# Kernel tuning notes

Hardware: AMD Instinct MI355X
Metric: run time of the kernel (lower is better)

Reference implementation:

```python
import jax, jax.numpy as jnp
import numpy as np

IN_F = 4096
OUT_F = 11008
GROUPSIZE = 128
N_GROUPS = IN_F // GROUPSIZE  # 32


def setup_inputs() -> dict:
    key = jax.random.key(0)
    k1, k2, k3, k4 = jax.random.split(key, 4)
    x = jax.random.normal(k1, (4, 2048, IN_F), dtype=jnp.float32)
    # packed 4-bit weights: 8 nibbles per int32 along the input dim
    qweight = jax.random.randint(k2, (IN_F // 8, OUT_F), 0, 2**31 - 1, dtype=jnp.int32)
    # packed 4-bit zero points: 8 nibbles per int32 along the output dim
    qzeros = jax.random.randint(k3, (N_GROUPS, OUT_F // 8), 0, 2**31 - 1, dtype=jnp.int32)
    scales = jax.random.uniform(k4, (N_GROUPS, OUT_F), dtype=jnp.float32,
                                minval=0.001, maxval=0.01)
    g_idx = (jnp.arange(IN_F, dtype=jnp.int32) // GROUPSIZE).astype(jnp.int32)
    return {"x": x, "qweight": qweight, "scales": scales,
            "qzeros": qzeros, "g_idx": g_idx}


def _dequantize(qweight, scales, qzeros, g_idx):
    """GPTQ v2 dequant: W[i, j] = scales[g_idx[i], j] * (q[i, j] - (z[g_idx[i], j] + 1))."""
    shifts = jnp.arange(8, dtype=jnp.int32) * 4  # nibble shift amounts
    # unpack weights along input dim: [in/8, 8, out] -> [in, out]
    q = (qweight[:, None, :] >> shifts[None, :, None]) & 0xF
    q = q.reshape(-1, qweight.shape[1]).astype(scales.dtype)
    # unpack zeros along output dim: [g, out/8, 8] -> [g, out]; +1 per GPTQ v2
    z = ((qzeros[:, :, None] >> shifts[None, None, :]) & 0xF) + 1
    z = z.reshape(qzeros.shape[0], -1).astype(scales.dtype)
    return scales[g_idx] * (q - z[g_idx])  # [in, out]


def reference(x, qweight, scales, qzeros, g_idx):
    W = _dequantize(qweight, scales, qzeros, g_idx)  # [IN_F, OUT_F]
    return jnp.einsum('bsi,io->bso', x, W)
```

## Files before the change

kernel.cpp:

```cpp
#include <hip/hip_runtime.h>
#include <hip/hip_bf16.h>

#define IN_F 4096
#define OUT_F 11008

typedef __bf16 bf16_t;
typedef bf16_t bf16x8 __attribute__((ext_vector_type(8)));
typedef float f32x4 __attribute__((ext_vector_type(4)));
typedef unsigned int u32;

__global__ __launch_bounds__(256) void cvt_x_kernel(const float* __restrict__ x,
                                                    bf16_t* __restrict__ xb) {
    size_t i = ((size_t)blockIdx.x * 256 + threadIdx.x) * 8;
    f32x4 v0 = *(const f32x4*)(x + i);
    f32x4 v1 = *(const f32x4*)(x + i + 4);
    bf16x8 h;
    h[0]=(bf16_t)v0[0]; h[1]=(bf16_t)v0[1]; h[2]=(bf16_t)v0[2]; h[3]=(bf16_t)v0[3];
    h[4]=(bf16_t)v1[0]; h[5]=(bf16_t)v1[1]; h[6]=(bf16_t)v1[2]; h[7]=(bf16_t)v1[3];
    *(bf16x8*)(xb + i) = h;
}

__global__ __launch_bounds__(256) void dequant_kernel(const int* __restrict__ qweight,
                                                      const float* __restrict__ scales,
                                                      const int* __restrict__ qzeros,
                                                      bf16_t* __restrict__ wt) {
    const int n   = blockIdx.x * 256 + threadIdx.x;
    const int kw0 = blockIdx.y * 4;
    const int g   = kw0 >> 4;
    const float s  = scales[(size_t)g * OUT_F + n];
    const int   zw = qzeros[(size_t)g * (OUT_F / 8) + (n >> 3)];
    const float nsz = -s * (float)(((zw >> ((n & 7) * 4)) & 0xF) + 1);
    bf16_t* dst = wt + (size_t)n * IN_F + kw0 * 8;
    #pragma unroll
    for (int j = 0; j < 4; ++j) {
        const int w = qweight[(size_t)(kw0 + j) * OUT_F + n];
        bf16x8 h;
        #pragma unroll
        for (int b = 0; b < 8; ++b)
            h[b] = (bf16_t)fmaf((float)((w >> (4 * b)) & 0xF), s, nsz);
        *(bf16x8*)(dst + j * 8) = h;
    }
}


#define NI (IN_F / 128)

__global__ __launch_bounds__(512, 2) void gemm_8ph(const bf16_t* __restrict__ A,
                                                   const bf16_t* __restrict__ B,
                                                   float* __restrict__ C) {
    __shared__ __align__(16) bf16_t smemA[2 * 2 * 128 * 64];
    __shared__ __align__(16) bf16_t smemB[2 * 2 * 128 * 64];

    const int tid  = threadIdx.x;
    const int lane = tid & 63;
    const int wid  = tid >> 6;
    const int wr   = wid >> 2;
    const int wc   = wid & 3;

    const int bid = blockIdx.x;
    const int swz = (bid & 7) * 172 + (bid >> 3);
    const int bx = swz % 43;
    const int by = swz / 43;
    const int m0 = by * 256;
    const int n0 = bx * 256;

    int lr0, kb0, lr1, kb1;
    {
        int L0 = tid * 16;
        int p0 = L0 ^ (((L0 >> 7) & 7) << 4);
        lr0 = p0 >> 7; kb0 = (p0 & 127) >> 1;
        int L1 = (512 + tid) * 16;
        int p1 = L1 ^ (((L1 >> 7) & 7) << 4);
        lr1 = p1 >> 7; kb1 = (p1 & 127) >> 1;
    }

    const int xm = (lane & 7) << 4;
    const int arow = lane & 15;
    int colk[2];
    #pragma unroll
    for (int ks = 0; ks < 2; ++ks)
        colk[ks] = ((ks * 64) + ((lane >> 4) * 16)) ^ xm;

#define STAGE(smem, buf, half, src, rbase, koff)                                           \
    do {                                                                                   \
        const bf16_t* g0_ = (src) + (size_t)((rbase) + lr0) * IN_F + (koff) + kb0;         \
        __builtin_amdgcn_global_load_lds(                                                  \
            (const __attribute__((address_space(1))) u32*)g0_,                             \
            (__attribute__((address_space(3))) u32*)((char*)(smem) + (buf) * 32768 +       \
                                                     (half) * 16384 + wid * 1024),         \
            16, 0, 0);                                                                     \
        const bf16_t* g1_ = (src) + (size_t)((rbase) + lr1) * IN_F + (koff) + kb1;         \
        __builtin_amdgcn_global_load_lds(                                                  \
            (const __attribute__((address_space(1))) u32*)g1_,                             \
            (__attribute__((address_space(3))) u32*)((char*)(smem) + (buf) * 32768 +       \
                                                     (half) * 16384 + 8192 + wid * 1024),  \
            16, 0, 0);                                                                     \
    } while (0)

#define STAGE_A(buf, half, koff) STAGE(smemA, buf, half, A, m0 + (half) * 128, koff)
#define STAGE_B(buf, half, koff) STAGE(smemB, buf, half, B, n0 + (half) * 128, koff)

#define LOAD_A(buf, mbase)                                                                 \
    _Pragma("unroll") for (int mm = 0; mm < 4; ++mm)                                       \
    _Pragma("unroll") for (int ks = 0; ks < 2; ++ks)                                       \
        aR[mm * 2 + ks] = *(const bf16x8*)((const char*)smemA + (buf) * 32768 +            \
            wr * 16384 + (((mbase) + mm) * 16 + arow) * 128 + colk[ks]);

#define LOAD_B(buf)                                                                        \
    _Pragma("unroll") for (int nn = 0; nn < 4; ++nn)                                       \
    _Pragma("unroll") for (int ks = 0; ks < 2; ++ks)                                       \
        bR[nn * 2 + ks] = *(const bf16x8*)((const char*)smemB + (buf) * 32768 +            \
            (wc >> 1) * 16384 + ((wc & 1) * 64 + nn * 16 + arow) * 128 + colk[ks]);

#define MFMA_Q(mbase, nbase)                                                               \
    __builtin_amdgcn_s_setprio(1);                                                         \
    _Pragma("unroll") for (int mm = 0; mm < 4; ++mm)                                       \
    _Pragma("unroll") for (int nn = 0; nn < 2; ++nn)                                       \
    _Pragma("unroll") for (int ks = 0; ks < 2; ++ks)                                       \
        acc[(mbase) + mm][(nbase) + nn] = __builtin_amdgcn_mfma_f32_16x16x32_bf16(         \
            aR[mm * 2 + ks], bR[((nbase) + nn) * 2 + ks], acc[(mbase) + mm][(nbase) + nn], \
            0, 0, 0);                                                                      \
    __builtin_amdgcn_s_setprio(0);

#define BAR() __builtin_amdgcn_s_barrier()
#define VMCNT6() asm volatile("s_waitcnt vmcnt(6)" ::: "memory")
#define VMCNT0() asm volatile("s_waitcnt vmcnt(0)" ::: "memory")

    f32x4 acc[8][4];
    #pragma unroll
    for (int m = 0; m < 8; ++m)
        #pragma unroll
        for (int n = 0; n < 4; ++n)
            acc[m][n] = (f32x4)0.0f;

    bf16x8 aR[8], bR[8];

    STAGE_B(0, 0, 0);  STAGE_B(0, 1, 0);
    STAGE_A(0, 0, 0);  STAGE_A(0, 1, 0);
    STAGE_B(1, 0, 64); STAGE_B(1, 1, 64);
    STAGE_A(1, 0, 64);
    VMCNT6();
    BAR();

    for (int i = 0; i < NI; ++i) {
        const int  kc = i * 128;
        const int  kn = kc + 128;
        const bool nl = (i + 1 < NI);

        LOAD_A(0, 0); LOAD_B(0);
        STAGE_A(1, 1, kc + 64);
        BAR();
        MFMA_Q(0, 0);
        BAR();
        if (nl) STAGE_B(0, 0, kn);
        BAR();
        MFMA_Q(0, 2);
        BAR();
        LOAD_A(0, 4);
        if (nl) STAGE_B(0, 1, kn);
        BAR();
        MFMA_Q(4, 0);
        BAR();
        if (nl) STAGE_A(0, 0, kn);
        BAR();
        MFMA_Q(4, 2);
        if (nl) VMCNT6(); else VMCNT0();
        BAR();
        LOAD_A(1, 0); LOAD_B(1);
        if (nl) STAGE_A(0, 1, kn);
        BAR();
        MFMA_Q(0, 0);
        BAR();
        if (nl) STAGE_B(1, 0, kc + 192);
        BAR();
        MFMA_Q(0, 2);
        BAR();
        LOAD_A(1, 4);
        if (nl) STAGE_B(1, 1, kc + 192);
        BAR();
        MFMA_Q(4, 0);
        BAR();
        if (nl) STAGE_A(1, 0, kc + 192);
        BAR();
        MFMA_Q(4, 2);
        if (nl) VMCNT6();
        BAR();
    }

    const int cn  = lane & 15;
    const int cr4 = (lane >> 4) * 4;
    #pragma unroll
    for (int m = 0; m < 8; ++m) {
        #pragma unroll
        for (int r = 0; r < 4; ++r) {
            const int grow = m0 + wr * 128 + m * 16 + cr4 + r;
            float* orow = C + (size_t)grow * OUT_F + n0 + wc * 64 + cn;
            #pragma unroll
            for (int n = 0; n < 4; ++n)
                orow[n * 16] = acc[m][n][r];
        }
    }
}

#define BMf 128
#define BNf 128
#define BKf 32
#define LDPF 40

__global__ __launch_bounds__(256, 2) void gptq_gemm_fused(
    const float* __restrict__ x, const int* __restrict__ qweight,
    const float* __restrict__ scales, const int* __restrict__ qzeros,
    float* __restrict__ out)
{
    __shared__ bf16_t As[BMf * LDPF];
    __shared__ bf16_t Bs[BNf * LDPF];
    const int tid = threadIdx.x, lane = tid & 63, wid = tid >> 6;
    const int wr = wid >> 1, wc = wid & 1;
    const int m0 = blockIdx.y * BMf, n0 = blockIdx.x * BNf;
    const int a_row = tid >> 2, a_slot = tid & 3;
    const int b_k8l = tid >> 7, b_n = tid & 127;

    f32x4 acc[4][4];
    #pragma unroll
    for (int i = 0; i < 4; ++i)
        #pragma unroll
        for (int j = 0; j < 4; ++j) acc[i][j] = (f32x4)0.0f;

    for (int kt = 0; kt < IN_F / BKf; ++kt) {
        const int k0 = kt * BKf;
        const int g  = k0 >> 7;
        __syncthreads();
        #pragma unroll
        for (int p = 0; p < 2; ++p) {
            const int row = a_row + p * 64;
            const float* src = x + (size_t)(m0 + row) * IN_F + k0 + a_slot * 8;
            f32x4 v0 = *(const f32x4*)src;
            f32x4 v1 = *(const f32x4*)(src + 4);
            bf16x8 h;
            h[0]=(bf16_t)v0[0]; h[1]=(bf16_t)v0[1]; h[2]=(bf16_t)v0[2]; h[3]=(bf16_t)v0[3];
            h[4]=(bf16_t)v1[0]; h[5]=(bf16_t)v1[1]; h[6]=(bf16_t)v1[2]; h[7]=(bf16_t)v1[3];
            *(bf16x8*)(&As[row * LDPF + a_slot * 8]) = h;
        }
        {
            const int gn = n0 + b_n;
            const float s  = scales[(size_t)g * OUT_F + gn];
            const int   zw = qzeros[(size_t)g * (OUT_F / 8) + (gn >> 3)];
            const float sz = s * (float)(((zw >> ((gn & 7) * 4)) & 0xF) + 1);
            #pragma unroll
            for (int p = 0; p < 2; ++p) {
                const int k8l = b_k8l + p * 2;
                const int w = qweight[(size_t)(k0 / 8 + k8l) * OUT_F + gn];
                bf16x8 h;
                #pragma unroll
                for (int j = 0; j < 8; ++j)
                    h[j] = (bf16_t)fmaf((float)((w >> (4 * j)) & 0xF), s, -sz);
                *(bf16x8*)(&Bs[b_n * LDPF + k8l * 8]) = h;
            }
        }
        __syncthreads();
        bf16x8 af[4], bfr[4];
        #pragma unroll
        for (int m = 0; m < 4; ++m)
            af[m] = *(const bf16x8*)(&As[(wr * 64 + m * 16 + (lane & 15)) * LDPF + (lane >> 4) * 8]);
        #pragma unroll
        for (int n = 0; n < 4; ++n)
            bfr[n] = *(const bf16x8*)(&Bs[(wc * 64 + n * 16 + (lane & 15)) * LDPF + (lane >> 4) * 8]);
        #pragma unroll
        for (int m = 0; m < 4; ++m)
            #pragma unroll
            for (int n = 0; n < 4; ++n)
                acc[m][n] = __builtin_amdgcn_mfma_f32_16x16x32_bf16(af[m], bfr[n], acc[m][n], 0, 0, 0);
    }
    const int cn = lane & 15, cr4 = (lane >> 4) * 4;
    #pragma unroll
    for (int m = 0; m < 4; ++m)
        #pragma unroll
        for (int r = 0; r < 4; ++r) {
            const int grow = m0 + wr * 64 + m * 16 + cr4 + r;
            float* orow = out + (size_t)grow * OUT_F + n0 + wc * 64 + cn;
            #pragma unroll
            for (int n = 0; n < 4; ++n) orow[n * 16] = acc[m][n][r];
        }
}

extern "C" void kernel_launch(void* const* d_in, const int* in_sizes, int n_in,
                              void* d_out, int out_size, void* d_ws, size_t ws_size,
                              hipStream_t stream) {
    const float* x       = (const float*)d_in[0];
    const int*   qweight = (const int*)d_in[1];
    const float* scales  = (const float*)d_in[2];
    const int*   qzeros  = (const int*)d_in[3];
    float* out = (float*)d_out;

    const int M = in_sizes[0] / IN_F;
    const size_t xb_bytes = (size_t)M * IN_F * 2;
    const size_t wt_bytes = (size_t)IN_F * OUT_F * 2;

    if (ws_size >= xb_bytes + wt_bytes && (M % 256) == 0) {
        bf16_t* xb = (bf16_t*)d_ws;
        bf16_t* wt = (bf16_t*)((char*)d_ws + xb_bytes);
        cvt_x_kernel<<<dim3((M * IN_F) / (256 * 8)), dim3(256), 0, stream>>>(x, xb);
        dequant_kernel<<<dim3(OUT_F / 256, IN_F / 32), dim3(256), 0, stream>>>(
            qweight, scales, qzeros, wt);
        const int nwg = (OUT_F / 256) * (M / 256);
        gemm_8ph<<<dim3(nwg), dim3(512), 0, stream>>>(xb, wt, out);
    } else {
        gptq_gemm_fused<<<dim3(OUT_F / BNf, M / BMf), dim3(256), 0, stream>>>(
            x, qweight, scales, qzeros, out);
    }
}
```

Measured before the change: 878.4 us.

## Double-buffer LDS register fragments to overlap ds_reads with MFMA phases

Result: slower. 1.301 ms (+48.2%).

```diff
diff --git a/kernel.cpp b/kernel.cpp
--- a/kernel.cpp
+++ b/kernel.cpp
@@ -100,30 +100,31 @@
 #define STAGE_A(buf, half, koff) STAGE(smemA, buf, half, A, m0 + (half) * 128, koff)
 #define STAGE_B(buf, half, koff) STAGE(smemB, buf, half, B, n0 + (half) * 128, koff)
 
-#define LOAD_A(buf, mbase)                                                                 \
+#define LOAD_A_FRAGS(dst, buf, mbase)                                                      \
     _Pragma("unroll") for (int mm = 0; mm < 4; ++mm)                                       \
     _Pragma("unroll") for (int ks = 0; ks < 2; ++ks)                                       \
-        aR[mm * 2 + ks] = *(const bf16x8*)((const char*)smemA + (buf) * 32768 +            \
+        dst[mm * 2 + ks] = *(const bf16x8*)((const char*)smemA + (buf) * 32768 +           \
             wr * 16384 + (((mbase) + mm) * 16 + arow) * 128 + colk[ks]);
 
-#define LOAD_B(buf)                                                                        \
-    _Pragma("unroll") for (int nn = 0; nn < 4; ++nn)                                       \
+#define LOAD_B_PAIR(dst, buf, P)                                                           \
+    _Pragma("unroll") for (int nn = 0; nn < 2; ++nn)                                       \
     _Pragma("unroll") for (int ks = 0; ks < 2; ++ks)                                       \
-        bR[nn * 2 + ks] = *(const bf16x8*)((const char*)smemB + (buf) * 32768 +            \
-            (wc >> 1) * 16384 + ((wc & 1) * 64 + nn * 16 + arow) * 128 + colk[ks]);
-
-#define MFMA_Q(mbase, nbase)                                                               \
+        dst[nn * 2 + ks] = *(const bf16x8*)((const char*)smemB + (buf) * 32768 +           \
+            (wc >> 1) * 16384 + ((wc & 1) * 64 + ((P) * 2 + nn) * 16 + arow) * 128 +       \
+            colk[ks]);
+
+#define MFMA_Q(aArr, bArr, mbase, nbase)                                                   \
     __builtin_amdgcn_s_setprio(1);                                                         \
     _Pragma("unroll") for (int mm = 0; mm < 4; ++mm)                                       \
     _Pragma("unroll") for (int nn = 0; nn < 2; ++nn)                                       \
     _Pragma("unroll") for (int ks = 0; ks < 2; ++ks)                                       \
         acc[(mbase) + mm][(nbase) + nn] = __builtin_amdgcn_mfma_f32_16x16x32_bf16(         \
-            aR[mm * 2 + ks], bR[((nbase) + nn) * 2 + ks], acc[(mbase) + mm][(nbase) + nn], \
+            aArr[mm * 2 + ks], bArr[nn * 2 + ks], acc[(mbase) + mm][(nbase) + nn],         \
             0, 0, 0);                                                                      \
     __builtin_amdgcn_s_setprio(0);
 
 #define BAR() __builtin_amdgcn_s_barrier()
-#define VMCNT6() asm volatile("s_waitcnt vmcnt(6)" ::: "memory")
+#define VMCNT4() asm volatile("s_waitcnt vmcnt(4)" ::: "memory")
 #define VMCNT0() asm volatile("s_waitcnt vmcnt(0)" ::: "memory")
 
     f32x4 acc[8][4];
@@ -133,57 +134,65 @@
         for (int n = 0; n < 4; ++n)
             acc[m][n] = (f32x4)0.0f;
 
-    bf16x8 aR[8], bR[8];
+    bf16x8 aM0[8], aM1[8], b01[4], b23[4];
 
     STAGE_B(0, 0, 0);  STAGE_B(0, 1, 0);
     STAGE_A(0, 0, 0);  STAGE_A(0, 1, 0);
     STAGE_B(1, 0, 64); STAGE_B(1, 1, 64);
     STAGE_A(1, 0, 64);
-    VMCNT6();
+    asm volatile("s_waitcnt vmcnt(6)" ::: "memory");
     BAR();
+    LOAD_A_FRAGS(aM0, 0, 0);
+    LOAD_B_PAIR(b01, 0, 0);
 
     for (int i = 0; i < NI; ++i) {
         const int  kc = i * 128;
         const int  kn = kc + 128;
         const bool nl = (i + 1 < NI);
 
-        LOAD_A(0, 0); LOAD_B(0);
+        LOAD_B_PAIR(b23, 0, 1);
         STAGE_A(1, 1, kc + 64);
         BAR();
-        MFMA_Q(0, 0);
-        BAR();
+        MFMA_Q(aM0, b01, 0, 0);
+        BAR();
+        LOAD_A_FRAGS(aM1, 0, 4);
         if (nl) STAGE_B(0, 0, kn);
         BAR();
-        MFMA_Q(0, 2);
-        BAR();
-        LOAD_A(0, 4);
+        MFMA_Q(aM0, b23, 0, 2);
+        BAR();
         if (nl) STAGE_B(0, 1, kn);
         BAR();
-        MFMA_Q(4, 0);
-        BAR();
+        MFMA_Q(aM1, b01, 4, 0);
+        if (nl) VMCNT4(); else VMCNT0();
+        BAR();
+        LOAD_A_FRAGS(aM0, 1, 0);
+        LOAD_B_PAIR(b01, 1, 0);
         if (nl) STAGE_A(0, 0, kn);
         BAR();
-        MFMA_Q(4, 2);
-        if (nl) VMCNT6(); else VMCNT0();
-        BAR();
-        LOAD_A(1, 0); LOAD_B(1);
+        MFMA_Q(aM1, b23, 4, 2);
+        BAR();
+        LOAD_B_PAIR(b23, 1, 1);
         if (nl) STAGE_A(0, 1, kn);
         BAR();
-        MFMA_Q(0, 0);
-        BAR();
+        MFMA_Q(aM0, b01, 0, 0);
+        BAR();
+        LOAD_A_FRAGS(aM1, 1, 4);
         if (nl) STAGE_B(1, 0, kc + 192);
         BAR();
-        MFMA_Q(0, 2);
-        BAR();
-        LOAD_A(1, 4);
+        MFMA_Q(aM0, b23, 0, 2);
+        BAR();
         if (nl) STAGE_B(1, 1, kc + 192);
         BAR();
-        MFMA_Q(4, 0);
-        BAR();
-        if (nl) STAGE_A(1, 0, kc + 192);
-        BAR();
-        MFMA_Q(4, 2);
-        if (nl) VMCNT6();
+        MFMA_Q(aM1, b01, 4, 0);
+        if (nl) VMCNT4();
+        BAR();
+        if (nl) {
+            LOAD_A_FRAGS(aM0, 0, 0);
+            LOAD_B_PAIR(b01, 0, 0);
+            STAGE_A(1, 0, kc + 192);
+        }
+        BAR();
+        MFMA_Q(aM1, b23, 4, 2);
         BAR();
     }
 
```
